# Optimization experiments

Hardware: AMD Instinct MI355X
Metric: run time of the kernel (lower is better)

## Reference

```python
import jax, jax.numpy as jnp
import numpy as np

B, S, E = 4, 2048, 1024
H, DK, DV = 16, 64, 64
LN_EPS = 1e-5
NEG = -1e9


def setup_inputs() -> dict:
    key = jax.random.key(0)
    ks = jax.random.split(key, 8)
    scale = 0.02
    return {
        "input_Q": jax.random.normal(ks[0], (B, S, E), jnp.float32),
        "input_K": jax.random.normal(ks[1], (B, S, E), jnp.float32),
        "input_V": jax.random.normal(ks[2], (B, S, E), jnp.float32),
        "attn_mask": jnp.zeros((B, S, S), jnp.bool_),
        "W_Q": jax.random.normal(ks[3], (E, H * DK), jnp.float32) * scale,
        "W_K": jax.random.normal(ks[4], (E, H * DK), jnp.float32) * scale,
        "W_V": jax.random.normal(ks[5], (E, H * DV), jnp.float32) * scale,
        "W_O": jax.random.normal(ks[6], (H * DV, E), jnp.float32) * scale,
        "ln_gamma": jnp.ones((E,), jnp.float32),
        "ln_beta": jnp.zeros((E,), jnp.float32),
    }


def reference(input_Q, input_K, input_V, attn_mask, W_Q, W_K, W_V, W_O, ln_gamma, ln_beta):
    # project and split heads: [B, S, E] -> [B, H, S, d]
    Q = (input_Q @ W_Q).reshape(B, S, H, DK).transpose(0, 2, 1, 3)
    K = (input_K @ W_K).reshape(B, S, H, DK).transpose(0, 2, 1, 3)
    V = (input_V @ W_V).reshape(B, S, H, DV).transpose(0, 2, 1, 3)

    # scaled dot-product attention with mask: scores [B, H, S, S]
    scores = jnp.einsum("bhqd,bhkd->bhqk", Q, K) / np.sqrt(DK).astype(np.float32)
    scores = jnp.where(attn_mask[:, None, :, :], NEG, scores)
    attn = jax.nn.softmax(scores, axis=-1)
    context = jnp.einsum("bhqk,bhkd->bhqd", attn, V)

    # merge heads and output projection
    context = context.transpose(0, 2, 1, 3).reshape(B, S, H * DV)
    output = context @ W_O

    # residual + LayerNorm over last dim
    x = output + input_Q
    mu = jnp.mean(x, axis=-1, keepdims=True)
    var = jnp.mean(jnp.square(x - mu), axis=-1, keepdims=True)
    out = (x - mu) * jax.lax.rsqrt(var + LN_EPS) * ln_gamma + ln_beta
    return (out, attn)
```

## Files before the change

kernel.cpp:

```cpp
#include <hip/hip_runtime.h>

typedef __attribute__((ext_vector_type(8))) short short8;
typedef __attribute__((ext_vector_type(4))) float f32x4;
typedef __attribute__((ext_vector_type(4))) unsigned short us4;
typedef __attribute__((ext_vector_type(8))) unsigned short us8;

#define SLEN 2048
#define EDIM 1024
#define NH 16
#define HD 64

__device__ __forceinline__ unsigned short f2bf(float x) {
    unsigned int u = __builtin_bit_cast(unsigned int, x);
    u += 0x7FFFu + ((u >> 16) & 1u);
    return (unsigned short)(u >> 16);
}

__global__ __launch_bounds__(256) void k_f32_to_bf16(const float* __restrict__ in,
                                                     unsigned short* __restrict__ out, int n4) {
    int i = blockIdx.x * blockDim.x + threadIdx.x;
    int stride = gridDim.x * blockDim.x;
    for (; i < n4; i += stride) {
        float4 v = ((const float4*)in)[i];
        us4 o;
        o.x = f2bf(v.x); o.y = f2bf(v.y); o.z = f2bf(v.z); o.w = f2bf(v.w);
        ((us4*)out)[i] = o;
    }
}

__global__ void k_transpose_bf16(const float* __restrict__ W, unsigned short* __restrict__ Wt) {
    __shared__ float tile[32][33];
    int x = blockIdx.x * 32 + threadIdx.x;
    for (int i = threadIdx.y; i < 32; i += 8)
        tile[i][threadIdx.x] = W[(size_t)(blockIdx.y * 32 + i) * EDIM + x];
    __syncthreads();
    int xo = blockIdx.y * 32 + threadIdx.x;
    for (int i = threadIdx.y; i < 32; i += 8)
        Wt[(size_t)(blockIdx.x * 32 + i) * EDIM + xo] = f2bf(tile[threadIdx.x][i]);
}

__global__ __launch_bounds__(256) void k_gemm_qkv(
    const unsigned short* __restrict__ Xq, const unsigned short* __restrict__ Xk,
    const unsigned short* __restrict__ Xv, const unsigned short* __restrict__ Wqt,
    const unsigned short* __restrict__ Wkt, const unsigned short* __restrict__ Wvt,
    unsigned short* __restrict__ Qh, unsigned short* __restrict__ Kh,
    unsigned short* __restrict__ Vth) {
    constexpr int LDT = 40;
    __shared__ __attribute__((aligned(16))) unsigned short sA[128 * LDT];
    __shared__ __attribute__((aligned(16))) unsigned short sB[128 * LDT];
    int z = blockIdx.z;
    const unsigned short* X = (z == 0) ? Xq : ((z == 1) ? Xk : Xv);
    const unsigned short* Wt = (z == 0) ? Wqt : ((z == 1) ? Wkt : Wvt);
    int tid = threadIdx.x, lane = tid & 63, wave = tid >> 6;
    int l16 = lane & 15, g4 = lane >> 4;
    int wm = (wave >> 1) * 64, wn = (wave & 1) * 64;
    int m0 = blockIdx.y * 128, n0 = blockIdx.x * 128;
    f32x4 acc[4][4] = {};
    for (int k0 = 0; k0 < EDIM; k0 += 32) {
        __syncthreads();
#pragma unroll
        for (int i = 0; i < 2; i++) {
            int u = tid + i * 256;
            int r = u >> 2, c = (u & 3) * 8;
            *(us8*)(sA + r * LDT + c) = *(const us8*)(X + (size_t)(m0 + r) * EDIM + k0 + c);
            *(us8*)(sB + r * LDT + c) = *(const us8*)(Wt + (size_t)(n0 + r) * EDIM + k0 + c);
        }
        __syncthreads();
        short8 a[4], b[4];
#pragma unroll
        for (int mi = 0; mi < 4; mi++)
            a[mi] = *(const short8*)(sA + (wm + mi * 16 + l16) * LDT + g4 * 8);
#pragma unroll
        for (int ni = 0; ni < 4; ni++)
            b[ni] = *(const short8*)(sB + (wn + ni * 16 + l16) * LDT + g4 * 8);
#pragma unroll
        for (int mi = 0; mi < 4; mi++)
#pragma unroll
            for (int ni = 0; ni < 4; ni++)
                acc[mi][ni] =
                    __builtin_amdgcn_mfma_f32_16x16x32_bf16(a[mi], b[ni], acc[mi][ni], 0, 0, 0);
    }
    float scale = (z == 0) ? 0.125f : 1.0f;
#pragma unroll
    for (int mi = 0; mi < 4; mi++) {
        int mbase = m0 + wm + mi * 16 + g4 * 4;
#pragma unroll
        for (int ni = 0; ni < 4; ni++) {
            int n = n0 + wn + ni * 16 + l16;
            int h = n >> 6, d = n & 63;
            if (z < 2) {
                unsigned short* O = (z == 0) ? Qh : Kh;
#pragma unroll
                for (int r = 0; r < 4; r++) {
                    int m = mbase + r;
                    int bb = m >> 11, s = m & (SLEN - 1);
                    O[(((size_t)bb * NH + h) * SLEN + s) * HD + d] = f2bf(acc[mi][ni][r] * scale);
                }
            } else {
                int bb = mbase >> 11, s0 = mbase & (SLEN - 1);
                us4 pk;
                pk.x = f2bf(acc[mi][ni][0]);
                pk.y = f2bf(acc[mi][ni][1]);
                pk.z = f2bf(acc[mi][ni][2]);
                pk.w = f2bf(acc[mi][ni][3]);
                *(us4*)(Vth + (((size_t)bb * NH + h) * HD + d) * SLEN + s0) = pk;
            }
        }
    }
}

__global__ __launch_bounds__(256) void k_attn(
    const unsigned short* __restrict__ Qh, const unsigned short* __restrict__ Kh,
    const unsigned short* __restrict__ Vth, const unsigned char* __restrict__ mask,
    float* __restrict__ attn, unsigned short* __restrict__ Ctx) {
    __shared__ __attribute__((aligned(16))) unsigned short sK[64 * 80];
    __shared__ __attribute__((aligned(16))) unsigned short sV[64 * 80];
    __shared__ __attribute__((aligned(16))) unsigned short sP[4][16 * 80];
    __shared__ uint4 sM4[64 * 4];
    unsigned char* sM = (unsigned char*)sM4;
    int tid = threadIdx.x, lane = tid & 63, wave = tid >> 6;
    int l16 = lane & 15, g4 = lane >> 4;
    int bh = blockIdx.y, b = bh >> 4, h = bh & 15;
    int q0 = blockIdx.x * 64;
    int qw = q0 + wave * 16;
    const unsigned short* Qbase = Qh + ((size_t)bh * SLEN + qw + l16) * HD;
    short8 aq0 = *(const short8*)(Qbase + g4 * 8);
    short8 aq1 = *(const short8*)(Qbase + 32 + g4 * 8);
    const size_t mbase = (size_t)b * SLEN * SLEN;
    float rs[4] = {0.f, 0.f, 0.f, 0.f};

    for (int kb = 0; kb < SLEN / 64; kb++) {
        int key0 = kb * 64;
        __syncthreads();
#pragma unroll
        for (int i = 0; i < 2; i++) {
            int u = tid + i * 256;
            int r = u >> 3, c = (u & 7) * 8;
            *(us8*)(sK + r * 80 + c) = *(const us8*)(Kh + ((size_t)bh * SLEN + key0 + r) * HD + c);
        }
        {
            int r = tid >> 2, c = (tid & 3) * 16;
            *(uint4*)(sM + r * 64 + c) = *(const uint4*)(mask + mbase + (size_t)(q0 + r) * SLEN + key0 + c);
        }
        __syncthreads();
#pragma unroll
        for (int ni = 0; ni < 4; ni++) {
            short8 b0 = *(const short8*)(sK + (ni * 16 + l16) * 80 + g4 * 8);
            short8 b1 = *(const short8*)(sK + (ni * 16 + l16) * 80 + 32 + g4 * 8);
            f32x4 c4 = {0.f, 0.f, 0.f, 0.f};
            c4 = __builtin_amdgcn_mfma_f32_16x16x32_bf16(aq0, b0, c4, 0, 0, 0);
            c4 = __builtin_amdgcn_mfma_f32_16x16x32_bf16(aq1, b1, c4, 0, 0, 0);
#pragma unroll
            for (int r = 0; r < 4; r++) {
                int qr = g4 * 4 + r;
                float p = sM[(wave * 16 + qr) * 64 + ni * 16 + l16] ? 0.0f : __expf(c4[r]);
                rs[r] += p;
            }
        }
    }
#pragma unroll
    for (int r = 0; r < 4; r++) {
        float v = rs[r];
        v += __shfl_xor(v, 1, 64);
        v += __shfl_xor(v, 2, 64);
        v += __shfl_xor(v, 4, 64);
        v += __shfl_xor(v, 8, 64);
        rs[r] = 1.0f / v;
    }

    f32x4 accd[4] = {};
    for (int kb = 0; kb < SLEN / 64; kb++) {
        int key0 = kb * 64;
        __syncthreads();
#pragma unroll
        for (int i = 0; i < 2; i++) {
            int u = tid + i * 256;
            int r = u >> 3, c = (u & 7) * 8;
            *(us8*)(sK + r * 80 + c) = *(const us8*)(Kh + ((size_t)bh * SLEN + key0 + r) * HD + c);
            *(us8*)(sV + r * 80 + c) = *(const us8*)(Vth + ((size_t)bh * HD + r) * SLEN + key0 + c);
        }
        {
            int r = tid >> 2, c = (tid & 3) * 16;
            *(uint4*)(sM + r * 64 + c) = *(const uint4*)(mask + mbase + (size_t)(q0 + r) * SLEN + key0 + c);
        }
        __syncthreads();
#pragma unroll
        for (int ni = 0; ni < 4; ni++) {
            short8 b0 = *(const short8*)(sK + (ni * 16 + l16) * 80 + g4 * 8);
            short8 b1 = *(const short8*)(sK + (ni * 16 + l16) * 80 + 32 + g4 * 8);
            f32x4 c4 = {0.f, 0.f, 0.f, 0.f};
            c4 = __builtin_amdgcn_mfma_f32_16x16x32_bf16(aq0, b0, c4, 0, 0, 0);
            c4 = __builtin_amdgcn_mfma_f32_16x16x32_bf16(aq1, b1, c4, 0, 0, 0);
#pragma unroll
            for (int r = 0; r < 4; r++) {
                int qr = g4 * 4 + r;
                float p = sM[(wave * 16 + qr) * 64 + ni * 16 + l16] ? 0.0f
                                                                   : __expf(c4[r]) * rs[r];
                attn[((size_t)bh * SLEN + qw + qr) * SLEN + key0 + ni * 16 + l16] = p;
                sP[wave][qr * 80 + ni * 16 + l16] = f2bf(p);
            }
        }
        short8 ap0 = *(const short8*)(&sP[wave][0] + l16 * 80 + g4 * 8);
        short8 ap1 = *(const short8*)(&sP[wave][0] + l16 * 80 + 32 + g4 * 8);
#pragma unroll
        for (int nd = 0; nd < 4; nd++) {
            short8 v0 = *(const short8*)(sV + (nd * 16 + l16) * 80 + g4 * 8);
            short8 v1 = *(const short8*)(sV + (nd * 16 + l16) * 80 + 32 + g4 * 8);
            accd[nd] = __builtin_amdgcn_mfma_f32_16x16x32_bf16(ap0, v0, accd[nd], 0, 0, 0);
            accd[nd] = __builtin_amdgcn_mfma_f32_16x16x32_bf16(ap1, v1, accd[nd], 0, 0, 0);
        }
    }
#pragma unroll
    for (int nd = 0; nd < 4; nd++)
#pragma unroll
        for (int r = 0; r < 4; r++) {
            int s = qw + g4 * 4 + r;
            Ctx[((size_t)b * SLEN + s) * EDIM + h * HD + nd * 16 + l16] = f2bf(accd[nd][r]);
        }
}

__global__ __launch_bounds__(256) void k_gemm_out(const unsigned short* __restrict__ Ctx,
                                                  const unsigned short* __restrict__ Wot,
                                                  const float* __restrict__ resid,
                                                  float* __restrict__ xout) {
    constexpr int LDT = 40;
    __shared__ __attribute__((aligned(16))) unsigned short sA[128 * LDT];
    __shared__ __attribute__((aligned(16))) unsigned short sB[128 * LDT];
    int tid = threadIdx.x, lane = tid & 63, wave = tid >> 6;
    int l16 = lane & 15, g4 = lane >> 4;
    int wm = (wave >> 1) * 64, wn = (wave & 1) * 64;
    int m0 = blockIdx.y * 128, n0 = blockIdx.x * 128;
    f32x4 acc[4][4] = {};
    for (int k0 = 0; k0 < EDIM; k0 += 32) {
        __syncthreads();
#pragma unroll
        for (int i = 0; i < 2; i++) {
            int u = tid + i * 256;
            int r = u >> 2, c = (u & 3) * 8;
            *(us8*)(sA + r * LDT + c) = *(const us8*)(Ctx + (size_t)(m0 + r) * EDIM + k0 + c);
            *(us8*)(sB + r * LDT + c) = *(const us8*)(Wot + (size_t)(n0 + r) * EDIM + k0 + c);
        }
        __syncthreads();
        short8 a[4], b[4];
#pragma unroll
        for (int mi = 0; mi < 4; mi++)
            a[mi] = *(const short8*)(sA + (wm + mi * 16 + l16) * LDT + g4 * 8);
#pragma unroll
        for (int ni = 0; ni < 4; ni++)
            b[ni] = *(const short8*)(sB + (wn + ni * 16 + l16) * LDT + g4 * 8);
#pragma unroll
        for (int mi = 0; mi < 4; mi++)
#pragma unroll
            for (int ni = 0; ni < 4; ni++)
                acc[mi][ni] =
                    __builtin_amdgcn_mfma_f32_16x16x32_bf16(a[mi], b[ni], acc[mi][ni], 0, 0, 0);
    }
#pragma unroll
    for (int mi = 0; mi < 4; mi++)
#pragma unroll
        for (int ni = 0; ni < 4; ni++)
#pragma unroll
            for (int r = 0; r < 4; r++) {
                int m = m0 + wm + mi * 16 + g4 * 4 + r;
                int n = n0 + wn + ni * 16 + l16;
                size_t idx = (size_t)m * EDIM + n;
                xout[idx] = acc[mi][ni][r] + resid[idx];
            }
}

__global__ __launch_bounds__(256) void k_ln(const float* __restrict__ x,
                                            const float* __restrict__ gamma,
                                            const float* __restrict__ beta,
                                            float* __restrict__ out) {
    int row = blockIdx.x, tid = threadIdx.x, lane = tid & 63, wave = tid >> 6;
    float4 v = ((const float4*)(x + (size_t)row * EDIM))[tid];
    float s = v.x + v.y + v.z + v.w;
    float ss = v.x * v.x + v.y * v.y + v.z * v.z + v.w * v.w;
#pragma unroll
    for (int m = 1; m < 64; m <<= 1) {
        s += __shfl_xor(s, m, 64);
        ss += __shfl_xor(ss, m, 64);
    }
    __shared__ float as[4], ass[4];
    if (lane == 0) { as[wave] = s; ass[wave] = ss; }
    __syncthreads();
    float sum = as[0] + as[1] + as[2] + as[3];
    float ssum = ass[0] + ass[1] + ass[2] + ass[3];
    float mean = sum * (1.0f / EDIM);
    float var = ssum * (1.0f / EDIM) - mean * mean;
    float rstd = rsqrtf(var + 1e-5f);
    float4 g = ((const float4*)gamma)[tid];
    float4 bt = ((const float4*)beta)[tid];
    float4 o;
    o.x = (v.x - mean) * rstd * g.x + bt.x;
    o.y = (v.y - mean) * rstd * g.y + bt.y;
    o.z = (v.z - mean) * rstd * g.z + bt.z;
    o.w = (v.w - mean) * rstd * g.w + bt.w;
    ((float4*)(out + (size_t)row * EDIM))[tid] = o;
}

extern "C" void kernel_launch(void* const* d_in, const int* in_sizes, int n_in, void* d_out,
                              int out_size, void* d_ws, size_t ws_size, hipStream_t stream) {
    const float* inQ = (const float*)d_in[0];
    const float* inK = (const float*)d_in[1];
    const float* inV = (const float*)d_in[2];
    const unsigned char* mask = (const unsigned char*)d_in[3];
    const float* WQ = (const float*)d_in[4];
    const float* WK = (const float*)d_in[5];
    const float* WV = (const float*)d_in[6];
    const float* WO = (const float*)d_in[7];
    const float* gamma = (const float*)d_in[8];
    const float* beta = (const float*)d_in[9];
    float* out = (float*)d_out;
    float* attn = out + (size_t)4 * SLEN * EDIM;
    char* ws = (char*)d_ws;

    unsigned short* Xq = (unsigned short*)(ws);
    unsigned short* Xk = (unsigned short*)(ws + 16777216);
    unsigned short* Xv = (unsigned short*)(ws + 2 * 16777216);
    unsigned short* Wqt = (unsigned short*)(ws + 3 * 16777216);
    unsigned short* Wkt = Wqt + 1048576;
    unsigned short* Wvt = Wkt + 1048576;
    unsigned short* Wot = Wvt + 1048576;
    unsigned short* Qh = (unsigned short*)(ws + 3 * 16777216 + 4 * 2097152);
    unsigned short* Kh = Qh + 8388608;
    unsigned short* Vth = Kh + 8388608;
    unsigned short* Ctx = Xq;
    float* xout = (float*)(ws + 16777216);

    int n4 = (4 * SLEN * EDIM) / 4;
    k_f32_to_bf16<<<2048, 256, 0, stream>>>(inQ, Xq, n4);
    k_f32_to_bf16<<<2048, 256, 0, stream>>>(inK, Xk, n4);
    k_f32_to_bf16<<<2048, 256, 0, stream>>>(inV, Xv, n4);
    dim3 tb(32, 8);
    k_transpose_bf16<<<dim3(32, 32), tb, 0, stream>>>(WQ, Wqt);
    k_transpose_bf16<<<dim3(32, 32), tb, 0, stream>>>(WK, Wkt);
    k_transpose_bf16<<<dim3(32, 32), tb, 0, stream>>>(WV, Wvt);
    k_transpose_bf16<<<dim3(32, 32), tb, 0, stream>>>(WO, Wot);
    k_gemm_qkv<<<dim3(8, 64, 3), 256, 0, stream>>>(Xq, Xk, Xv, Wqt, Wkt, Wvt, Qh, Kh, Vth);
    k_attn<<<dim3(SLEN / 64, 4 * NH), 256, 0, stream>>>(Qh, Kh, Vth, mask, attn, Ctx);
    k_gemm_out<<<dim3(8, 64), 256, 0, stream>>>(Ctx, Wot, inQ, xout);
    k_ln<<<4 * SLEN, 256, 0, stream>>>(xout, gamma, beta, out);
}
```

Before: 1.760 ms.

## Double attention query tile per block and use direct global-to-LDS loads in GEMMs

The attention kernel now processes 128 queries per block (32 per wave, two 16-row sub-tiles). Each K/V tile loaded into shared memory is therefore reused across twice as many queries, halving K/V reloads and launching half as many blocks. The QKV and output GEMMs now use global_load_lds to stage tiles straight into unpadded shared memory, skipping the register round-trip. The trade-offs are more register pressure in attention, and possible LDS bank conflicts from the unpadded 32-element row stride.

```diff
diff --git a/kernel.cpp b/kernel.cpp
--- a/kernel.cpp
+++ b/kernel.cpp
@@ -14,6 +14,12 @@
     unsigned int u = __builtin_bit_cast(unsigned int, x);
     u += 0x7FFFu + ((u >> 16) & 1u);
     return (unsigned short)(u >> 16);
+}
+
+__device__ __forceinline__ void gload16(const unsigned short* g, unsigned short* l) {
+    __builtin_amdgcn_global_load_lds(
+        (const __attribute__((address_space(1))) unsigned int*)g,
+        (__attribute__((address_space(3))) unsigned int*)l, 16, 0, 0);
 }
 
 __global__ __launch_bounds__(256) void k_f32_to_bf16(const float* __restrict__ in,
@@ -45,9 +51,8 @@
     const unsigned short* __restrict__ Wkt, const unsigned short* __restrict__ Wvt,
     unsigned short* __restrict__ Qh, unsigned short* __restrict__ Kh,
     unsigned short* __restrict__ Vth) {
-    constexpr int LDT = 40;
-    __shared__ __attribute__((aligned(16))) unsigned short sA[128 * LDT];
-    __shared__ __attribute__((aligned(16))) unsigned short sB[128 * LDT];
+    __shared__ __attribute__((aligned(16))) unsigned short sA[128 * 32];
+    __shared__ __attribute__((aligned(16))) unsigned short sB[128 * 32];
     int z = blockIdx.z;
     const unsigned short* X = (z == 0) ? Xq : ((z == 1) ? Xk : Xv);
     const unsigned short* Wt = (z == 0) ? Wqt : ((z == 1) ? Wkt : Wvt);
@@ -55,24 +60,25 @@
     int l16 = lane & 15, g4 = lane >> 4;
     int wm = (wave >> 1) * 64, wn = (wave & 1) * 64;
     int m0 = blockIdx.y * 128, n0 = blockIdx.x * 128;
+    int sr = lane >> 2, sc = (lane & 3) * 8;
     f32x4 acc[4][4] = {};
     for (int k0 = 0; k0 < EDIM; k0 += 32) {
         __syncthreads();
 #pragma unroll
         for (int i = 0; i < 2; i++) {
-            int u = tid + i * 256;
-            int r = u >> 2, c = (u & 3) * 8;
-            *(us8*)(sA + r * LDT + c) = *(const us8*)(X + (size_t)(m0 + r) * EDIM + k0 + c);
-            *(us8*)(sB + r * LDT + c) = *(const us8*)(Wt + (size_t)(n0 + r) * EDIM + k0 + c);
+            int c = wave * 2 + i;
+            int r = c * 16 + sr;
+            gload16(X + (size_t)(m0 + r) * EDIM + k0 + sc, sA + c * 512);
+            gload16(Wt + (size_t)(n0 + r) * EDIM + k0 + sc, sB + c * 512);
         }
         __syncthreads();
         short8 a[4], b[4];
 #pragma unroll
         for (int mi = 0; mi < 4; mi++)
-            a[mi] = *(const short8*)(sA + (wm + mi * 16 + l16) * LDT + g4 * 8);
+            a[mi] = *(const short8*)(sA + (wm + mi * 16 + l16) * 32 + g4 * 8);
 #pragma unroll
         for (int ni = 0; ni < 4; ni++)
-            b[ni] = *(const short8*)(sB + (wn + ni * 16 + l16) * LDT + g4 * 8);
+            b[ni] = *(const short8*)(sB + (wn + ni * 16 + l16) * 32 + g4 * 8);
 #pragma unroll
         for (int mi = 0; mi < 4; mi++)
 #pragma unroll
@@ -116,18 +122,21 @@
     __shared__ __attribute__((aligned(16))) unsigned short sK[64 * 80];
     __shared__ __attribute__((aligned(16))) unsigned short sV[64 * 80];
     __shared__ __attribute__((aligned(16))) unsigned short sP[4][16 * 80];
-    __shared__ uint4 sM4[64 * 4];
-    unsigned char* sM = (unsigned char*)sM4;
+    __shared__ __attribute__((aligned(16))) unsigned char sM[128 * 64];
     int tid = threadIdx.x, lane = tid & 63, wave = tid >> 6;
     int l16 = lane & 15, g4 = lane >> 4;
     int bh = blockIdx.y, b = bh >> 4, h = bh & 15;
-    int q0 = blockIdx.x * 64;
-    int qw = q0 + wave * 16;
+    int q0 = blockIdx.x * 128;
+    int qw = q0 + wave * 32;
     const unsigned short* Qbase = Qh + ((size_t)bh * SLEN + qw + l16) * HD;
-    short8 aq0 = *(const short8*)(Qbase + g4 * 8);
-    short8 aq1 = *(const short8*)(Qbase + 32 + g4 * 8);
+    short8 aq[2][2];
+#pragma unroll
+    for (int s = 0; s < 2; s++) {
+        aq[s][0] = *(const short8*)(Qbase + s * 16 * HD + g4 * 8);
+        aq[s][1] = *(const short8*)(Qbase + s * 16 * HD + 32 + g4 * 8);
+    }
     const size_t mbase = (size_t)b * SLEN * SLEN;
-    float rs[4] = {0.f, 0.f, 0.f, 0.f};
+    float rs[2][4] = {};
 
     for (int kb = 0; kb < SLEN / 64; kb++) {
         int key0 = kb * 64;
@@ -139,36 +148,43 @@
             *(us8*)(sK + r * 80 + c) = *(const us8*)(Kh + ((size_t)bh * SLEN + key0 + r) * HD + c);
         }
         {
-            int r = tid >> 2, c = (tid & 3) * 16;
-            *(uint4*)(sM + r * 64 + c) = *(const uint4*)(mask + mbase + (size_t)(q0 + r) * SLEN + key0 + c);
+            int r = tid >> 1, c = (tid & 1) * 32;
+            const unsigned char* mp = mask + mbase + (size_t)(q0 + r) * SLEN + key0 + c;
+            *(uint4*)(sM + r * 64 + c) = *(const uint4*)(mp);
+            *(uint4*)(sM + r * 64 + c + 16) = *(const uint4*)(mp + 16);
         }
         __syncthreads();
 #pragma unroll
         for (int ni = 0; ni < 4; ni++) {
             short8 b0 = *(const short8*)(sK + (ni * 16 + l16) * 80 + g4 * 8);
             short8 b1 = *(const short8*)(sK + (ni * 16 + l16) * 80 + 32 + g4 * 8);
-            f32x4 c4 = {0.f, 0.f, 0.f, 0.f};
-            c4 = __builtin_amdgcn_mfma_f32_16x16x32_bf16(aq0, b0, c4, 0, 0, 0);
-            c4 = __builtin_amdgcn_mfma_f32_16x16x32_bf16(aq1, b1, c4, 0, 0, 0);
-#pragma unroll
-            for (int r = 0; r < 4; r++) {
-                int qr = g4 * 4 + r;
-                float p = sM[(wave * 16 + qr) * 64 + ni * 16 + l16] ? 0.0f : __expf(c4[r]);
-                rs[r] += p;
-            }
-        }
-    }
-#pragma unroll
-    for (int r = 0; r < 4; r++) {
-        float v = rs[r];
-        v += __shfl_xor(v, 1, 64);
-        v += __shfl_xor(v, 2, 64);
-        v += __shfl_xor(v, 4, 64);
-        v += __shfl_xor(v, 8, 64);
-        rs[r] = 1.0f / v;
-    }
-
-    f32x4 accd[4] = {};
+#pragma unroll
+            for (int s = 0; s < 2; s++) {
+                f32x4 c4 = {0.f, 0.f, 0.f, 0.f};
+                c4 = __builtin_amdgcn_mfma_f32_16x16x32_bf16(aq[s][0], b0, c4, 0, 0, 0);
+                c4 = __builtin_amdgcn_mfma_f32_16x16x32_bf16(aq[s][1], b1, c4, 0, 0, 0);
+#pragma unroll
+                for (int r = 0; r < 4; r++) {
+                    int row = wave * 32 + s * 16 + g4 * 4 + r;
+                    float p = sM[row * 64 + ni * 16 + l16] ? 0.0f : __expf(c4[r]);
+                    rs[s][r] += p;
+                }
+            }
+        }
+    }
+#pragma unroll
+    for (int s = 0; s < 2; s++)
+#pragma unroll
+        for (int r = 0; r < 4; r++) {
+            float v = rs[s][r];
+            v += __shfl_xor(v, 1, 64);
+            v += __shfl_xor(v, 2, 64);
+            v += __shfl_xor(v, 4, 64);
+            v += __shfl_xor(v, 8, 64);
+            rs[s][r] = 1.0f / v;
+        }
+
+    f32x4 accd[2][4] = {};
     for (int kb = 0; kb < SLEN / 64; kb++) {
         int key0 = kb * 64;
         __syncthreads();
@@ -180,74 +196,83 @@
             *(us8*)(sV + r * 80 + c) = *(const us8*)(Vth + ((size_t)bh * HD + r) * SLEN + key0 + c);
         }
         {
-            int r = tid >> 2, c = (tid & 3) * 16;
-            *(uint4*)(sM + r * 64 + c) = *(const uint4*)(mask + mbase + (size_t)(q0 + r) * SLEN + key0 + c);
-        }
-        __syncthreads();
-#pragma unroll
-        for (int ni = 0; ni < 4; ni++) {
-            short8 b0 = *(const short8*)(sK + (ni * 16 + l16) * 80 + g4 * 8);
-            short8 b1 = *(const short8*)(sK + (ni * 16 + l16) * 80 + 32 + g4 * 8);
-            f32x4 c4 = {0.f, 0.f, 0.f, 0.f};
-            c4 = __builtin_amdgcn_mfma_f32_16x16x32_bf16(aq0, b0, c4, 0, 0, 0);
-            c4 = __builtin_amdgcn_mfma_f32_16x16x32_bf16(aq1, b1, c4, 0, 0, 0);
+            int r = tid >> 1, c = (tid & 1) * 32;
+            const unsigned char* mp = mask + mbase + (size_t)(q0 + r) * SLEN + key0 + c;
+            *(uint4*)(sM + r * 64 + c) = *(const uint4*)(mp);
+            *(uint4*)(sM + r * 64 + c + 16) = *(const uint4*)(mp + 16);
+        }
+        __syncthreads();
+#pragma unroll
+        for (int s = 0; s < 2; s++) {
+#pragma unroll
+            for (int ni = 0; ni < 4; ni++) {
+                short8 b0 = *(const short8*)(sK + (ni * 16 + l16) * 80 + g4 * 8);
+                short8 b1 = *(const short8*)(sK + (ni * 16 + l16) * 80 + 32 + g4 * 8);
+                f32x4 c4 = {0.f, 0.f, 0.f, 0.f};
+                c4 = __builtin_amdgcn_mfma_f32_16x16x32_bf16(aq[s][0], b0, c4, 0, 0, 0);
+                c4 = __builtin_amdgcn_mfma_f32_16x16x32_bf16(aq[s][1], b1, c4, 0, 0, 0);
+#pragma unroll
+                for (int r = 0; r < 4; r++) {
+                    int qr = g4 * 4 + r;
+                    int row = wave * 32 + s * 16 + qr;
+                    float p = sM[row * 64 + ni * 16 + l16] ? 0.0f
+                                                          : __expf(c4[r]) * rs[s][r];
+                    attn[((size_t)bh * SLEN + q0 + row) * SLEN + key0 + ni * 16 + l16] = p;
+                    sP[wave][qr * 80 + ni * 16 + l16] = f2bf(p);
+                }
+            }
+            short8 ap0 = *(const short8*)(&sP[wave][0] + l16 * 80 + g4 * 8);
+            short8 ap1 = *(const short8*)(&sP[wave][0] + l16 * 80 + 32 + g4 * 8);
+#pragma unroll
+            for (int nd = 0; nd < 4; nd++) {
+                short8 v0 = *(const short8*)(sV + (nd * 16 + l16) * 80 + g4 * 8);
+                short8 v1 = *(const short8*)(sV + (nd * 16 + l16) * 80 + 32 + g4 * 8);
+                accd[s][nd] = __builtin_amdgcn_mfma_f32_16x16x32_bf16(ap0, v0, accd[s][nd], 0, 0, 0);
+                accd[s][nd] = __builtin_amdgcn_mfma_f32_16x16x32_bf16(ap1, v1, accd[s][nd], 0, 0, 0);
+            }
+        }
+    }
+#pragma unroll
+    for (int s = 0; s < 2; s++)
+#pragma unroll
+        for (int nd = 0; nd < 4; nd++)
 #pragma unroll
             for (int r = 0; r < 4; r++) {
-                int qr = g4 * 4 + r;
-                float p = sM[(wave * 16 + qr) * 64 + ni * 16 + l16] ? 0.0f
-                                                                   : __expf(c4[r]) * rs[r];
-                attn[((size_t)bh * SLEN + qw + qr) * SLEN + key0 + ni * 16 + l16] = p;
-                sP[wave][qr * 80 + ni * 16 + l16] = f2bf(p);
-            }
-        }
-        short8 ap0 = *(const short8*)(&sP[wave][0] + l16 * 80 + g4 * 8);
-        short8 ap1 = *(const short8*)(&sP[wave][0] + l16 * 80 + 32 + g4 * 8);
-#pragma unroll
-        for (int nd = 0; nd < 4; nd++) {
-            short8 v0 = *(const short8*)(sV + (nd * 16 + l16) * 80 + g4 * 8);
-            short8 v1 = *(const short8*)(sV + (nd * 16 + l16) * 80 + 32 + g4 * 8);
-            accd[nd] = __builtin_amdgcn_mfma_f32_16x16x32_bf16(ap0, v0, accd[nd], 0, 0, 0);
-            accd[nd] = __builtin_amdgcn_mfma_f32_16x16x32_bf16(ap1, v1, accd[nd], 0, 0, 0);
-        }
-    }
-#pragma unroll
-    for (int nd = 0; nd < 4; nd++)
-#pragma unroll
-        for (int r = 0; r < 4; r++) {
-            int s = qw + g4 * 4 + r;
-            Ctx[((size_t)b * SLEN + s) * EDIM + h * HD + nd * 16 + l16] = f2bf(accd[nd][r]);
-        }
+                int srow = qw + s * 16 + g4 * 4 + r;
+                Ctx[((size_t)b * SLEN + srow) * EDIM + h * HD + nd * 16 + l16] =
+                    f2bf(accd[s][nd][r]);
+            }
 }
 
 __global__ __launch_bounds__(256) void k_gemm_out(const unsigned short* __restrict__ Ctx,
                                                   const unsigned short* __restrict__ Wot,
                                                   const float* __restrict__ resid,
                                                   float* __restrict__ xout) {
-    constexpr int LDT = 40;
-    __shared__ __attribute__((aligned(16))) unsigned short sA[128 * LDT];
-    __shared__ __attribute__((aligned(16))) unsigned short sB[128 * LDT];
+    __shared__ __attribute__((aligned(16))) unsigned short sA[128 * 32];
+    __shared__ __attribute__((aligned(16))) unsigned short sB[128 * 32];
     int tid = threadIdx.x, lane = tid & 63, wave = tid >> 6;
     int l16 = lane & 15, g4 = lane >> 4;
     int wm = (wave >> 1) * 64, wn = (wave & 1) * 64;
     int m0 = blockIdx.y * 128, n0 = blockIdx.x * 128;
+    int sr = lane >> 2, sc = (lane & 3) * 8;
     f32x4 acc[4][4] = {};
     for (int k0 = 0; k0 < EDIM; k0 += 32) {
         __syncthreads();
 #pragma unroll
         for (int i = 0; i < 2; i++) {
-            int u = tid + i * 256;
-            int r = u >> 2, c = (u & 3) * 8;
-            *(us8*)(sA + r * LDT + c) = *(const us8*)(Ctx + (size_t)(m0 + r) * EDIM + k0 + c);
-            *(us8*)(sB + r * LDT + c) = *(const us8*)(Wot + (size_t)(n0 + r) * EDIM + k0 + c);
+            int c = wave * 2 + i;
+            int r = c * 16 + sr;
+            gload16(Ctx + (size_t)(m0 + r) * EDIM + k0 + sc, sA + c * 512);
+            gload16(Wot + (size_t)(n0 + r) * EDIM + k0 + sc, sB + c * 512);
         }
         __syncthreads();
         short8 a[4], b[4];
 #pragma unroll
         for (int mi = 0; mi < 4; mi++)
-            a[mi] = *(const short8*)(sA + (wm + mi * 16 + l16) * LDT + g4 * 8);
+            a[mi] = *(const short8*)(sA + (wm + mi * 16 + l16) * 32 + g4 * 8);
 #pragma unroll
         for (int ni = 0; ni < 4; ni++)
-            b[ni] = *(const short8*)(sB + (wn + ni * 16 + l16) * LDT + g4 * 8);
+            b[ni] = *(const short8*)(sB + (wn + ni * 16 + l16) * 32 + g4 * 8);
 #pragma unroll
         for (int mi = 0; mi < 4; mi++)
 #pragma unroll
@@ -338,7 +363,7 @@
     k_transpose_bf16<<<dim3(32, 32), tb, 0, stream>>>(WV, Wvt);
     k_transpose_bf16<<<dim3(32, 32), tb, 0, stream>>>(WO, Wot);
     k_gemm_qkv<<<dim3(8, 64, 3), 256, 0, stream>>>(Xq, Xk, Xv, Wqt, Wkt, Wvt, Qh, Kh, Vth);
-    k_attn<<<dim3(SLEN / 64, 4 * NH), 256, 0, stream>>>(Qh, Kh, Vth, mask, attn, Ctx);
+    k_attn<<<dim3(SLEN / 128, 4 * NH), 256, 0, stream>>>(Qh, Kh, Vth, mask, attn, Ctx);
     k_gemm_out<<<dim3(8, 64), 256, 0, stream>>>(Ctx, Wot, inQ, xout);
     k_ln<<<4 * SLEN, 256, 0, stream>>>(xout, gamma, beta, out);
 }
```

Result: faster. 1.667 ms (-5.3%).
